# Optimization experiments

Hardware: AMD Instinct MI355X
Metric: run time of the kernel (lower is better)

## Reference

```python
import jax, jax.numpy as jnp
import numpy as np

DIM = 128
HEADS = 32
DIM_HEAD = 64
INNER = DIM * DIM_HEAD  # 8192, as written in the source (dim * dim_head)
D = INNER // HEADS      # 256 per-head dim
B, N = 1, 2048
ROT = 64                # partial rotary width (l)
SCALE = DIM ** (-0.5)   # source uses dim**-0.5, not head-dim


def _rotate_half(x):
    # x: [..., l]; split as (j d) with j=2 -> cat(-x2, x1)
    x1, x2 = jnp.split(x, 2, axis=-1)
    return jnp.concatenate((-x2, x1), axis=-1)


def _apply_rotary(q, k, freqs):
    # freqs: [n, l]; q,k: [b,h,n,d] with l <= d (partial rotary)
    l = freqs.shape[-1]
    cos, sin = jnp.cos(freqs), jnp.sin(freqs)  # broadcast over b,h
    ql, qr = q[..., :l], q[..., l:]
    kl, kr = k[..., :l], k[..., l:]
    ql = ql * cos + _rotate_half(ql) * sin
    kl = kl * cos + _rotate_half(kl) * sin
    return jnp.concatenate((ql, qr), axis=-1), jnp.concatenate((kl, kr), axis=-1)


def setup_inputs() -> dict:
    key = jax.random.key(0)
    k1, k2, k3, k4, k5 = jax.random.split(key, 5)
    return {
        "x": jax.random.normal(k1, (B, N, DIM), dtype=jnp.float32),
        "Wqkv": jax.random.normal(k2, (3 * INNER, DIM), dtype=jnp.float32) * 0.02,
        "Wproj": jax.random.normal(k3, (DIM, INNER), dtype=jnp.float32) * 0.02,
        "bproj": jax.random.normal(k4, (DIM,), dtype=jnp.float32) * 0.02,
        "rotary_pos_emb": jax.random.normal(k5, (N, ROT), dtype=jnp.float32),
    }


def reference(x, Wqkv, Wproj, bproj, rotary_pos_emb):
    b, n, _ = x.shape
    qkv = x @ Wqkv.T                                   # [b, n, 3*inner]
    qkv = qkv.reshape(b, n, 3, HEADS, D)               # (qkv h d) ordering
    qkv = jnp.transpose(qkv, (2, 0, 3, 1, 4))          # [3, b, h, n, d]
    q, k, v = qkv[0], qkv[1], qkv[2]
    q, k = _apply_rotary(q, k, rotary_pos_emb)
    energy = jnp.einsum("bhid,bhjd->bhij", q, k) * SCALE  # [b,h,n,n]
    attn = jax.nn.softmax(energy, axis=-1)
    out = jnp.einsum("bhij,bhjd->bhid", attn, v)       # [b,h,n,d]
    out = jnp.transpose(out, (0, 2, 1, 3)).reshape(b, n, INNER)
    return out @ Wproj.T + bproj
```

## Files before the change

### kernel.cpp

```cpp
#include <hip/hip_runtime.h>


typedef unsigned short u16;
typedef unsigned int u32;
typedef __attribute__((ext_vector_type(8))) u16 u16x8;
typedef __attribute__((ext_vector_type(8))) __bf16 bf16x8;
typedef __attribute__((ext_vector_type(4))) float f32x4;
typedef __attribute__((ext_vector_type(16))) float f32x16;
typedef __attribute__((ext_vector_type(4))) u32 u32x4;
typedef __attribute__((ext_vector_type(2))) u32 u32x2;

#define DEV static __device__ __forceinline__

DEV u16 f2b(float f) {
  __bf16 h = (__bf16)f;
  return __builtin_bit_cast(u16, h);
}
DEV float b2f(u16 b) {
  u32 u = ((u32)b) << 16;
  return __builtin_bit_cast(float, u);
}
DEV u32 pk2(float a, float b) { return (u32)f2b(a) | ((u32)f2b(b) << 16); }

DEV f32x4 mfma16(u16x8 a, u16x8 b, f32x4 c) {
  return __builtin_amdgcn_mfma_f32_16x16x32_bf16(
      __builtin_bit_cast(bf16x8, a), __builtin_bit_cast(bf16x8, b), c, 0, 0, 0);
}
DEV f32x16 mfma32(u16x8 a, u16x8 b, f32x16 c) {
  return __builtin_amdgcn_mfma_f32_32x32x16_bf16(
      __builtin_bit_cast(bf16x8, a), __builtin_bit_cast(bf16x8, b), c, 0, 0, 0);
}

DEV int swz(int row, int kelem, int rowBytes) {
  return row * rowBytes + ((kelem * 2) ^ ((row & 7) << 4));
}

DEV void dma16(const void* g, void* l) {
  __builtin_amdgcn_global_load_lds(
      (const __attribute__((address_space(1))) void*)g,
      (__attribute__((address_space(3))) void*)l, 16, 0, 0);
}

__global__ __launch_bounds__(256) void k_cvt(const float* __restrict__ src,
                                             u16* __restrict__ dst, int n8) {
  int i = blockIdx.x * 256 + threadIdx.x;
  if (i >= n8) return;
  const float4* s = (const float4*)src;
  float4 a = s[i * 2], b = s[i * 2 + 1];
  u16x8 o;
  o[0] = f2b(a.x); o[1] = f2b(a.y); o[2] = f2b(a.z); o[3] = f2b(a.w);
  o[4] = f2b(b.x); o[5] = f2b(b.y); o[6] = f2b(b.z); o[7] = f2b(b.w);
  *(u16x8*)(dst + (size_t)i * 8) = o;
}

__global__ __launch_bounds__(256) void k_qkv(const u16* __restrict__ xb,
                                             const u16* __restrict__ wb,
                                             u16* __restrict__ qw,
                                             u16* __restrict__ kw,
                                             u16* __restrict__ vw) {
  __shared__ char lds[65536];
  const int tid = threadIdx.x;
  const int rt = blockIdx.x % 192, nt = blockIdx.x / 192;
  const int r0 = rt * 128, n0 = nt * 128;
#pragma unroll
  for (int p = 0; p < 8; ++p) {
    int row = p * 16 + (tid >> 4);
    int k0 = (tid & 15) * 8;
    *(u16x8*)(lds + swz(row, k0, 256)) =
        *(const u16x8*)(wb + (size_t)(r0 + row) * 128 + k0);
    *(u16x8*)(lds + 32768 + swz(row, k0, 256)) =
        *(const u16x8*)(xb + (size_t)(n0 + row) * 128 + k0);
  }
  __syncthreads();
  const int wid = tid >> 6, lane = tid & 63, lq = lane & 15, g = lane >> 4;
  const int wr = wid >> 1, wn = wid & 1;
  const bool isV = (r0 >= 16384);
  f32x4 acc[4][4] = {};
#pragma unroll
  for (int ks = 0; ks < 4; ++ks) {
    u16x8 wa[4], xa[4];
#pragma unroll
    for (int i = 0; i < 4; ++i) {
      int rw = wr * 64 + i * 16 + lq;
      wa[i] = *(const u16x8*)(lds + swz(rw, ks * 32 + g * 8, 256));
      int rx = wn * 64 + i * 16 + lq;
      xa[i] = *(const u16x8*)(lds + 32768 + swz(rx, ks * 32 + g * 8, 256));
    }
    if (!isV) {
#pragma unroll
      for (int i = 0; i < 4; ++i)
#pragma unroll
        for (int j = 0; j < 4; ++j) acc[i][j] = mfma16(wa[i], xa[j], acc[i][j]);
    } else {
#pragma unroll
      for (int i = 0; i < 4; ++i)
#pragma unroll
        for (int j = 0; j < 4; ++j) acc[i][j] = mfma16(xa[j], wa[i], acc[i][j]);
    }
  }
  const float SMQ = 0.08838834764831845f * 1.4426950408889634f;
  if (!isV) {
#pragma unroll
    for (int i = 0; i < 4; ++i) {
      int rb = r0 + wr * 64 + i * 16 + g * 4;
      u16* dst0 = (rb >= 8192) ? kw : qw;
      float scl = (rb >= 8192) ? 1.0f : SMQ;
      int hd = rb & 8191;
      int h = hd >> 8, db = hd & 255;
#pragma unroll
      for (int j = 0; j < 4; ++j) {
        int n = n0 + wn * 64 + j * 16 + lq;
        u32x2 pk;
        pk.x = pk2(acc[i][j][0] * scl, acc[i][j][1] * scl);
        pk.y = pk2(acc[i][j][2] * scl, acc[i][j][3] * scl);
        *(u32x2*)(dst0 + ((size_t)h * 2048 + n) * 256 + db) = pk;
      }
    }
  } else {
#pragma unroll
    for (int i = 0; i < 4; ++i) {
      int rc = r0 - 16384 + wr * 64 + i * 16 + lq;
      int h = rc >> 8, d = rc & 255;
#pragma unroll
      for (int j = 0; j < 4; ++j) {
        int nb = n0 + wn * 64 + j * 16 + g * 4;
        u32x2 pk;
        pk.x = pk2(acc[i][j][0], acc[i][j][1]);
        pk.y = pk2(acc[i][j][2], acc[i][j][3]);
        *(u32x2*)(vw + ((size_t)h * 256 + d) * 2048 + nb) = pk;
      }
    }
  }
}

__global__ __launch_bounds__(256) void k_rope(u16* __restrict__ qw,
                                              u16* __restrict__ kw,
                                              const float* __restrict__ fr) {
  int idx = blockIdx.x * 256 + threadIdx.x;
  int seg = idx & 3;
  int n = (idx >> 2) & 2047;
  int h = (idx >> 13) & 31;
  u16* base = ((idx >> 18) ? kw : qw) + ((size_t)h * 2048 + n) * 256 + seg * 8;
  u16x8 lo = *(const u16x8*)base;
  u16x8 hi = *(const u16x8*)(base + 32);
  const float* f = fr + n * 64 + seg * 8;
  u16x8 nlo, nhi;
#pragma unroll
  for (int e = 0; e < 8; ++e) {
    float fl = f[e], fh = f[e + 32];
    float sl, cl, sh, ch;
    __sincosf(fl, &sl, &cl);
    __sincosf(fh, &sh, &ch);
    float a = b2f(lo[e]), b = b2f(hi[e]);
    nlo[e] = f2b(a * cl - b * sl);
    nhi[e] = f2b(b * ch + a * sh);
  }
  *(u16x8*)base = nlo;
  *(u16x8*)(base + 32) = nhi;
}

__global__ __launch_bounds__(512, 2) void k_attn(const u16* __restrict__ qw,
                                                 const u16* __restrict__ kw,
                                                 const u16* __restrict__ vw,
                                                 u16* __restrict__ ow) {
  __shared__ char lds[98304];
  const int tid = threadIdx.x;
  const int h = blockIdx.x & 31;
  const int qb = blockIdx.x >> 5;
  const int wid = tid >> 6, lane = tid & 63;
  const int l31 = lane & 31, h2 = lane >> 5;
  const int q0w = qb * 256 + wid * 32;
  const int lane16 = lane * 16;

  const u16* kbase = kw + (size_t)h * 2048 * 256;
  const u16* vbase = vw + (size_t)h * 256 * 2048;

  const bool isK = (wid < 4);
  const int dstslot = isK ? wid * 4 : 16 + (wid - 4) * 4;
  int off[4];
#pragma unroll
  for (int i = 0; i < 4; ++i) {
    if (isK) {
      int s = wid * 4 + i;
      off[i] = l31 * 256 + s * 16 + h2 * 8;
    } else {
      int u = (wid - 4) * 4 + i;
      off[i] = ((u >> 1) * 32 + l31) * 2048 + (u & 1) * 16 + h2 * 8;
    }
  }

  u16x8 qf[16];
  {
    const u16* qp = qw + ((size_t)h * 2048 + q0w + l31) * 256 + h2 * 8;
#pragma unroll
    for (int dt = 0; dt < 16; ++dt) qf[dt] = *(const u16x8*)(qp + dt * 16);
  }

  f32x16 oacc[8] = {};
  float mrun = -1e30f, lrun = 0.f;

#define STAGE(T, BUF)                                               \
  {                                                                 \
    const int kv0_ = (T) * 32;                                      \
    char* b_ = lds + (BUF) * 32768;                                 \
    if (isK) {                                                      \
      _Pragma("unroll") for (int i = 0; i < 4; ++i)                 \
          dma16(kbase + (size_t)kv0_ * 256 + off[i],                \
                b_ + (dstslot + i) * 1024);                         \
    } else {                                                        \
      _Pragma("unroll") for (int i = 0; i < 4; ++i)                 \
          dma16(vbase + kv0_ + off[i], b_ + (dstslot + i) * 1024);  \
    }                                                               \
  }

  STAGE(0, 0);
  STAGE(1, 1);
  int rb = 0, sb = 2;

  for (int t = 0; t < 64; ++t) {
    if (t < 63)
      asm volatile("s_waitcnt vmcnt(4)" ::: "memory");
    else
      asm volatile("s_waitcnt vmcnt(0)" ::: "memory");
    __builtin_amdgcn_s_barrier();
    asm volatile("" ::: "memory");
    if (t < 62) STAGE(t + 2, sb);

    const char* kb = lds + rb * 32768;

    f32x16 sa = {};
    __builtin_amdgcn_s_setprio(1);
#pragma unroll
    for (int dt = 0; dt < 16; ++dt) {
      u16x8 ka = *(const u16x8*)(kb + dt * 1024 + lane16);
      sa = mfma32(ka, qf[dt], sa);
    }
    __builtin_amdgcn_s_setprio(0);

    float m8[8];
#pragma unroll
    for (int r = 0; r < 8; ++r) m8[r] = fmaxf(sa[r], sa[r + 8]);
#pragma unroll
    for (int r = 0; r < 4; ++r) m8[r] = fmaxf(m8[r], m8[r + 4]);
    float mt = fmaxf(fmaxf(m8[0], m8[1]), fmaxf(m8[2], m8[3]));
    mt = fmaxf(mt, __shfl_xor(mt, 32));
    if (!__all(mt - mrun <= 8.0f)) {
      float mnew = fmaxf(mrun, mt);
      float corr = __builtin_amdgcn_exp2f(mrun - mnew);
      lrun *= corr;
#pragma unroll
      for (int dt = 0; dt < 8; ++dt)
#pragma unroll
        for (int r = 0; r < 16; ++r) oacc[dt][r] *= corr;
      mrun = mnew;
    }
    float p[16];
#pragma unroll
    for (int r = 0; r < 16; ++r)
      p[r] = __builtin_amdgcn_exp2f(sa[r] - mrun);
    float s8[8];
#pragma unroll
    for (int r = 0; r < 8; ++r) s8[r] = p[r] + p[r + 8];
#pragma unroll
    for (int r = 0; r < 4; ++r) s8[r] = s8[r] + s8[r + 4];
    float lt = (s8[0] + s8[1]) + (s8[2] + s8[3]);
    lt += __shfl_xor(lt, 32);
    lrun += lt;

    u32 pkk[8], xpk[8];
#pragma unroll
    for (int j = 0; j < 8; ++j) pkk[j] = pk2(p[2 * j], p[2 * j + 1]);
#pragma unroll
    for (int j = 0; j < 8; ++j) xpk[j] = (u32)__shfl_xor((int)pkk[j], 32);
    u32x4 b0v, b1v;
    b0v[0] = h2 ? xpk[2] : pkk[0];
    b0v[1] = h2 ? xpk[3] : pkk[1];
    b0v[2] = h2 ? pkk[2] : xpk[0];
    b0v[3] = h2 ? pkk[3] : xpk[1];
    b1v[0] = h2 ? xpk[6] : pkk[4];
    b1v[1] = h2 ? xpk[7] : pkk[5];
    b1v[2] = h2 ? pkk[6] : xpk[4];
    b1v[3] = h2 ? pkk[7] : xpk[5];
    u16x8 pb0 = __builtin_bit_cast(u16x8, b0v);
    u16x8 pb1 = __builtin_bit_cast(u16x8, b1v);

    __builtin_amdgcn_s_setprio(1);
#pragma unroll
    for (int dt = 0; dt < 8; ++dt) {
      u16x8 v0 = *(const u16x8*)(kb + 16384 + (dt * 2) * 1024 + lane16);
      oacc[dt] = mfma32(v0, pb0, oacc[dt]);
      u16x8 v1 = *(const u16x8*)(kb + 16384 + (dt * 2 + 1) * 1024 + lane16);
      oacc[dt] = mfma32(v1, pb1, oacc[dt]);
    }
    __builtin_amdgcn_s_setprio(0);

    rb = (rb == 2) ? 0 : rb + 1;
    sb = (sb == 2) ? 0 : sb + 1;
  }
#undef STAGE

  float inv = 1.0f / lrun;
  u16* orow = ow + (size_t)(q0w + l31) * 8192 + h * 256 + h2 * 4;
#pragma unroll
  for (int dt = 0; dt < 8; ++dt)
#pragma unroll
    for (int k = 0; k < 4; ++k) {
      u32x2 o2;
      o2.x = pk2(oacc[dt][4 * k] * inv, oacc[dt][4 * k + 1] * inv);
      o2.y = pk2(oacc[dt][4 * k + 2] * inv, oacc[dt][4 * k + 3] * inv);
      *(u32x2*)(orow + dt * 32 + k * 8) = o2;
    }
}

__global__ __launch_bounds__(256) void k_proj(const u16* __restrict__ ow,
                                              const u16* __restrict__ wp,
                                              float* __restrict__ part) {
  __shared__ char lds[49152];
  const int tid = threadIdx.x;
  const int nt = blockIdx.x >> 3, kc = blockIdx.x & 7;
  const int n0 = nt * 64, kb = kc * 1024;
  const int wid = tid >> 6, lane = tid & 63, lq = lane & 15, g = lane >> 4;
  f32x4 acc[8] = {};
  for (int kt = 0; kt < 8; ++kt) {
    int kk = kb + kt * 128;
#pragma unroll
    for (int p = 0; p < 4; ++p) {
      int nr = p * 16 + (tid >> 4);
      int k0 = (tid & 15) * 8;
      *(u16x8*)(lds + swz(nr, k0, 256)) =
          *(const u16x8*)(ow + (size_t)(n0 + nr) * 8192 + kk + k0);
    }
#pragma unroll
    for (int p = 0; p < 8; ++p) {
      int er = p * 16 + (tid >> 4);
      int k0 = (tid & 15) * 8;
      *(u16x8*)(lds + 16384 + swz(er, k0, 256)) =
          *(const u16x8*)(wp + (size_t)er * 8192 + kk + k0);
    }
    __syncthreads();
#pragma unroll
    for (int ks = 0; ks < 4; ++ks) {
      int nr = wid * 16 + lq;
      u16x8 oa = *(const u16x8*)(lds + swz(nr, ks * 32 + g * 8, 256));
#pragma unroll
      for (int ef = 0; ef < 8; ++ef) {
        int er = ef * 16 + lq;
        u16x8 wf = *(const u16x8*)(lds + 16384 + swz(er, ks * 32 + g * 8, 256));
        acc[ef] = mfma16(oa, wf, acc[ef]);
      }
    }
    __syncthreads();
  }
  float* pb = part + (size_t)kc * 262144;
#pragma unroll
  for (int ef = 0; ef < 8; ++ef)
#pragma unroll
    for (int r = 0; r < 4; ++r) {
      int n = n0 + wid * 16 + g * 4 + r;
      pb[n * 128 + ef * 16 + lq] = acc[ef][r];
    }
}

__global__ __launch_bounds__(256) void k_reduce(const float* __restrict__ part,
                                                const float* __restrict__ bias,
                                                float* __restrict__ out) {
  int i = blockIdx.x * 256 + threadIdx.x;
  float s = bias[i & 127];
#pragma unroll
  for (int c = 0; c < 8; ++c) s += part[(size_t)c * 262144 + i];
  out[i] = s;
}

extern "C" void kernel_launch(void* const* d_in, const int* in_sizes, int n_in,
                              void* d_out, int out_size, void* d_ws, size_t ws_size,
                              hipStream_t stream) {
  const float* x = (const float*)d_in[0];
  const float* wqkv = (const float*)d_in[1];
  const float* wproj = (const float*)d_in[2];
  const float* bproj = (const float*)d_in[3];
  const float* rope = (const float*)d_in[4];
  char* ws = (char*)d_ws;
  u16* xb    = (u16*)(ws);
  u16* wqkvb = (u16*)(ws + 524288);
  u16* wpb   = (u16*)(ws + 6815744);
  u16* qw    = (u16*)(ws + 8912896);
  u16* kw    = (u16*)(ws + 42467328);
  u16* vw    = (u16*)(ws + 76021760);
  u16* owv   = (u16*)(ws + 109576192);
  float* part = (float*)(ws + 8912896);

  k_cvt<<<128, 256, 0, stream>>>(x, xb, 32768);
  k_cvt<<<1536, 256, 0, stream>>>(wqkv, wqkvb, 393216);
  k_cvt<<<512, 256, 0, stream>>>(wproj, wpb, 131072);
  k_qkv<<<3072, 256, 0, stream>>>(xb, wqkvb, qw, kw, vw);
  k_rope<<<2048, 256, 0, stream>>>(qw, kw, rope);
  k_attn<<<256, 512, 0, stream>>>(qw, kw, vw, owv);
  k_proj<<<256, 256, 0, stream>>>(owv, wpb, part);
  k_reduce<<<1024, 256, 0, stream>>>(part, bproj, (float*)d_out);
}
```

Baseline: 229.4 us.

## Fuse fp32-to-bf16 conversion into GEMM loads and software-pipeline QK^T in attention

Removes the three separate conversion kernels and instead converts fp32 x, Wqkv and Wproj to bf16 while staging them into LDS inside the QKV and projection kernels. The attention loop is restructured so the QK^T for the next KV tile is computed before the softmax and PV of the current tile, with a three-buffer rotation (V, K, staging) and a full vmcnt(0) wait each iteration. This saves launches and an extra global round trip, but the GEMMs now read twice the bytes from global memory. The stricter wait in attention may expose load latency.

```diff
diff --git a/kernel.cpp b/kernel.cpp
--- a/kernel.cpp
+++ b/kernel.cpp
@@ -35,26 +35,21 @@
   return row * rowBytes + ((kelem * 2) ^ ((row & 7) << 4));
 }
 
+DEV u16x8 pk8(float4 a, float4 b) {
+  u16x8 o;
+  o[0] = f2b(a.x); o[1] = f2b(a.y); o[2] = f2b(a.z); o[3] = f2b(a.w);
+  o[4] = f2b(b.x); o[5] = f2b(b.y); o[6] = f2b(b.z); o[7] = f2b(b.w);
+  return o;
+}
+
 DEV void dma16(const void* g, void* l) {
   __builtin_amdgcn_global_load_lds(
       (const __attribute__((address_space(1))) void*)g,
       (__attribute__((address_space(3))) void*)l, 16, 0, 0);
 }
 
-__global__ __launch_bounds__(256) void k_cvt(const float* __restrict__ src,
-                                             u16* __restrict__ dst, int n8) {
-  int i = blockIdx.x * 256 + threadIdx.x;
-  if (i >= n8) return;
-  const float4* s = (const float4*)src;
-  float4 a = s[i * 2], b = s[i * 2 + 1];
-  u16x8 o;
-  o[0] = f2b(a.x); o[1] = f2b(a.y); o[2] = f2b(a.z); o[3] = f2b(a.w);
-  o[4] = f2b(b.x); o[5] = f2b(b.y); o[6] = f2b(b.z); o[7] = f2b(b.w);
-  *(u16x8*)(dst + (size_t)i * 8) = o;
-}
-
-__global__ __launch_bounds__(256) void k_qkv(const u16* __restrict__ xb,
-                                             const u16* __restrict__ wb,
+__global__ __launch_bounds__(256) void k_qkv(const float* __restrict__ x,
+                                             const float* __restrict__ wq,
                                              u16* __restrict__ qw,
                                              u16* __restrict__ kw,
                                              u16* __restrict__ vw) {
@@ -66,10 +61,12 @@
   for (int p = 0; p < 8; ++p) {
     int row = p * 16 + (tid >> 4);
     int k0 = (tid & 15) * 8;
+    const float* wsp = wq + (size_t)(r0 + row) * 128 + k0;
     *(u16x8*)(lds + swz(row, k0, 256)) =
-        *(const u16x8*)(wb + (size_t)(r0 + row) * 128 + k0);
+        pk8(*(const float4*)wsp, *(const float4*)(wsp + 4));
+    const float* xsp = x + (size_t)(n0 + row) * 128 + k0;
     *(u16x8*)(lds + 32768 + swz(row, k0, 256)) =
-        *(const u16x8*)(xb + (size_t)(n0 + row) * 128 + k0);
+        pk8(*(const float4*)xsp, *(const float4*)(xsp + 4));
   }
   __syncthreads();
   const int wid = tid >> 6, lane = tid & 63, lq = lane & 15, g = lane >> 4;
@@ -213,29 +210,40 @@
     }                                                               \
   }
 
+  auto QKT = [&](const char* kb_) {
+    f32x16 s = {};
+#pragma unroll
+    for (int dt = 0; dt < 16; ++dt) {
+      u16x8 ka = *(const u16x8*)(kb_ + dt * 1024 + lane16);
+      s = mfma32(ka, qf[dt], s);
+    }
+    return s;
+  };
+
   STAGE(0, 0);
   STAGE(1, 1);
-  int rb = 0, sb = 2;
+  asm volatile("s_waitcnt vmcnt(4)" ::: "memory");
+  __builtin_amdgcn_s_barrier();
+  asm volatile("" ::: "memory");
+
+  __builtin_amdgcn_s_setprio(1);
+  f32x16 sa = QKT(lds);
+  __builtin_amdgcn_s_setprio(0);
+
+  int vB = 0, kB = 1, sB = 2;
 
   for (int t = 0; t < 64; ++t) {
-    if (t < 63)
-      asm volatile("s_waitcnt vmcnt(4)" ::: "memory");
-    else
-      asm volatile("s_waitcnt vmcnt(0)" ::: "memory");
+    asm volatile("s_waitcnt vmcnt(0)" ::: "memory");
     __builtin_amdgcn_s_barrier();
     asm volatile("" ::: "memory");
-    if (t < 62) STAGE(t + 2, sb);
-
-    const char* kb = lds + rb * 32768;
-
-    f32x16 sa = {};
-    __builtin_amdgcn_s_setprio(1);
-#pragma unroll
-    for (int dt = 0; dt < 16; ++dt) {
-      u16x8 ka = *(const u16x8*)(kb + dt * 1024 + lane16);
-      sa = mfma32(ka, qf[dt], sa);
-    }
-    __builtin_amdgcn_s_setprio(0);
+    if (t < 62) STAGE(t + 2, sB);
+
+    f32x16 sn = sa;
+    if (t < 63) {
+      __builtin_amdgcn_s_setprio(1);
+      sn = QKT(lds + kB * 32768);
+      __builtin_amdgcn_s_setprio(0);
+    }
 
     float m8[8];
 #pragma unroll
@@ -284,18 +292,19 @@
     u16x8 pb0 = __builtin_bit_cast(u16x8, b0v);
     u16x8 pb1 = __builtin_bit_cast(u16x8, b1v);
 
+    const char* vb = lds + vB * 32768 + 16384;
     __builtin_amdgcn_s_setprio(1);
 #pragma unroll
     for (int dt = 0; dt < 8; ++dt) {
-      u16x8 v0 = *(const u16x8*)(kb + 16384 + (dt * 2) * 1024 + lane16);
+      u16x8 v0 = *(const u16x8*)(vb + (dt * 2) * 1024 + lane16);
       oacc[dt] = mfma32(v0, pb0, oacc[dt]);
-      u16x8 v1 = *(const u16x8*)(kb + 16384 + (dt * 2 + 1) * 1024 + lane16);
+      u16x8 v1 = *(const u16x8*)(vb + (dt * 2 + 1) * 1024 + lane16);
       oacc[dt] = mfma32(v1, pb1, oacc[dt]);
     }
     __builtin_amdgcn_s_setprio(0);
 
-    rb = (rb == 2) ? 0 : rb + 1;
-    sb = (sb == 2) ? 0 : sb + 1;
+    sa = sn;
+    int tmp = vB; vB = kB; kB = sB; sB = tmp;
   }
 #undef STAGE
 
@@ -313,7 +322,7 @@
 }
 
 __global__ __launch_bounds__(256) void k_proj(const u16* __restrict__ ow,
-                                              const u16* __restrict__ wp,
+                                              const float* __restrict__ wp,
                                               float* __restrict__ part) {
   __shared__ char lds[49152];
   const int tid = threadIdx.x;
@@ -334,8 +343,9 @@
     for (int p = 0; p < 8; ++p) {
       int er = p * 16 + (tid >> 4);
       int k0 = (tid & 15) * 8;
+      const float* wsp = wp + (size_t)er * 8192 + kk + k0;
       *(u16x8*)(lds + 16384 + swz(er, k0, 256)) =
-          *(const u16x8*)(wp + (size_t)er * 8192 + kk + k0);
+          pk8(*(const float4*)wsp, *(const float4*)(wsp + 4));
     }
     __syncthreads();
 #pragma unroll
@@ -380,21 +390,15 @@
   const float* bproj = (const float*)d_in[3];
   const float* rope = (const float*)d_in[4];
   char* ws = (char*)d_ws;
-  u16* xb    = (u16*)(ws);
-  u16* wqkvb = (u16*)(ws + 524288);
-  u16* wpb   = (u16*)(ws + 6815744);
-  u16* qw    = (u16*)(ws + 8912896);
-  u16* kw    = (u16*)(ws + 42467328);
-  u16* vw    = (u16*)(ws + 76021760);
-  u16* owv   = (u16*)(ws + 109576192);
-  float* part = (float*)(ws + 8912896);
-
-  k_cvt<<<128, 256, 0, stream>>>(x, xb, 32768);
-  k_cvt<<<1536, 256, 0, stream>>>(wqkv, wqkvb, 393216);
-  k_cvt<<<512, 256, 0, stream>>>(wproj, wpb, 131072);
-  k_qkv<<<3072, 256, 0, stream>>>(xb, wqkvb, qw, kw, vw);
+  u16* qw  = (u16*)(ws);
+  u16* kw  = (u16*)(ws + 33554432);
+  u16* vw  = (u16*)(ws + 67108864);
+  u16* owv = (u16*)(ws + 100663296);
+  float* part = (float*)ws;
+
+  k_qkv<<<3072, 256, 0, stream>>>(x, wqkv, qw, kw, vw);
   k_rope<<<2048, 256, 0, stream>>>(qw, kw, rope);
   k_attn<<<256, 512, 0, stream>>>(qw, kw, vw, owv);
-  k_proj<<<256, 256, 0, stream>>>(owv, wpb, part);
+  k_proj<<<256, 256, 0, stream>>>(owv, wproj, part);
   k_reduce<<<1024, 256, 0, stream>>>(part, bproj, (float*)d_out);
 }
```

Measured after the change: 246.7 us. 7.6% more time.
